# Optimization experiments

Hardware: AMD Instinct MI355X
Metric: run time of the kernel (lower is better)

Reference implementation:

```python
import jax, jax.numpy as jnp
import numpy as np
import math

B, D, S, H = 4, 1024, 2048, 16


def setup_inputs() -> dict:
    key = jax.random.key(0)
    ks = jax.random.split(key, 9)
    scale = 0.02
    return {
        "x": jax.random.normal(ks[0], (B, D, S), dtype=jnp.float32),
        "Wq": jax.random.normal(ks[1], (D, D), dtype=jnp.float32) * scale,
        "bq": jnp.zeros((D,), dtype=jnp.float32),
        "Wk": jax.random.normal(ks[2], (D, D), dtype=jnp.float32) * scale,
        "bk": jnp.zeros((D,), dtype=jnp.float32),
        "Wv": jax.random.normal(ks[3], (D, D), dtype=jnp.float32) * scale,
        "bv": jnp.zeros((D,), dtype=jnp.float32),
        "Wo": jax.random.normal(ks[4], (D, D), dtype=jnp.float32) * scale,
        "bo": jnp.zeros((D,), dtype=jnp.float32),
        "num_heads": H,
    }


def _positional_encoding(d_model, seq_len):
    # pe[0::2, :] = sin(pos * denom), pe[1::2, :] = cos(pos * denom)
    pos = jnp.arange(seq_len, dtype=jnp.float32)[None, :]            # [1, S]
    denom = jnp.exp(jnp.arange(0, d_model, 2, dtype=jnp.float32)
                    * (-math.log(10000.0) / d_model))[:, None]        # [D/2, 1]
    angles = pos * denom                                              # [D/2, S]
    pe = jnp.zeros((d_model, seq_len), dtype=jnp.float32)
    pe = pe.at[0::2, :].set(jnp.sin(angles))
    pe = pe.at[1::2, :].set(jnp.cos(angles))
    return pe


def reference(x, Wq, bq, Wk, bk, Wv, bv, Wo, bo, num_heads):
    b, d_model, s = x.shape
    head_dim = d_model // num_heads
    x = x + _positional_encoding(d_model, s)[None, :, :]  # broadcast over batch
    x = jnp.transpose(x, (0, 2, 1))                       # [B, S, D]
    q = x @ Wq.T + bq
    k = x @ Wk.T + bk
    v = x @ Wv.T + bv
    # [B, S, H, hd] -> [B, H, S, hd]
    q = q.reshape(b, s, num_heads, head_dim).transpose(0, 2, 1, 3)
    k = k.reshape(b, s, num_heads, head_dim).transpose(0, 2, 1, 3)
    v = v.reshape(b, s, num_heads, head_dim).transpose(0, 2, 1, 3)
    scores = jnp.einsum('bhqd,bhkd->bhqk', q, k) / jnp.sqrt(
        jnp.asarray(head_dim, dtype=jnp.float32))
    attn = jax.nn.softmax(scores, axis=-1)
    out = jnp.einsum('bhqk,bhkd->bhqd', attn, v)          # [B, H, S, hd]
    out = out.transpose(0, 2, 1, 3).reshape(b, s, d_model)
    out = out @ Wo.T + bo
    return jnp.transpose(out, (0, 2, 1))                  # [B, D, S]
```

## Files before the change

kernel.cpp:

```cpp
#include <hip/hip_runtime.h>


typedef __bf16 bf16;
typedef __attribute__((ext_vector_type(8))) __bf16 bf16x8;
typedef __attribute__((ext_vector_type(4))) __bf16 bf16x4;
typedef __attribute__((ext_vector_type(2))) __bf16 bf16x2;
typedef __attribute__((ext_vector_type(4))) float f32x4;
typedef __attribute__((ext_vector_type(2))) unsigned int uintx2;
typedef __attribute__((ext_vector_type(4))) unsigned int uintx4;

#define NB 4
#define ND 1024
#define NS 2048
#define NH 16
#define NM 8192

__device__ __forceinline__ void gld16(const void* g, void* l) {
  __builtin_amdgcn_global_load_lds((__attribute__((address_space(1))) void*)g,
                                   (__attribute__((address_space(3))) void*)l, 16, 0, 0);
}

__device__ __forceinline__ float exp2_fast(float x) {
#if __has_builtin(__builtin_amdgcn_exp2f)
  return __builtin_amdgcn_exp2f(x);
#else
  return exp2f(x);
#endif
}

__device__ __forceinline__ unsigned pk2(float a, float b) {
  bf16x2 t;
  t[0] = (bf16)a;
  t[1] = (bf16)b;
  return __builtin_bit_cast(unsigned int, t);
}

__device__ __forceinline__ void lane_xchg(unsigned a, unsigned b, unsigned& lo,
                                          unsigned& hi) {
#if __has_builtin(__builtin_amdgcn_permlane32_swap) && \
    __has_builtin(__builtin_amdgcn_permlane16_swap)
  uintx2 r = __builtin_amdgcn_permlane32_swap(a, b, false, false);
  uintx2 r2 = __builtin_amdgcn_permlane16_swap(r[0], r[1], false, false);
  lo = r2[0];
  hi = r2[1];
#else
  const int lane = threadIdx.x & 63;
  const int src = (lane & 15) + ((lane >> 4) & 1) * 32;
  const unsigned as = (unsigned)__shfl((int)a, src, 64);
  const unsigned bs = (unsigned)__shfl((int)b, src, 64);
  const unsigned as2 = (unsigned)__shfl((int)a, src + 16, 64);
  const unsigned bs2 = (unsigned)__shfl((int)b, src + 16, 64);
  lo = (lane >= 32) ? bs : as;
  hi = (lane >= 32) ? bs2 : as2;
#endif
}

__global__ __launch_bounds__(256) void prep_x_kernel(const float* __restrict__ x,
                                                     bf16* __restrict__ xT) {
  __shared__ float t[32][33];
  const int tx = threadIdx.x, ty = threadIdx.y;
  const int s0 = blockIdx.x * 32, d0 = blockIdx.y * 32, b = blockIdx.z;
#pragma unroll
  for (int i = 0; i < 4; ++i) {
    const int rr = ty + i * 8;
    const int d = d0 + rr, s = s0 + tx;
    const float freq = __expf(-(float)(d >> 1) * 0.01798894603980689f);
    const float ang = (float)s * freq;
    const float pe = (d & 1) ? cosf(ang) : sinf(ang);
    t[rr][tx] = x[((size_t)b * ND + d) * NS + s] + pe;
  }
  __syncthreads();
#pragma unroll
  for (int i = 0; i < 4; ++i) {
    const int a = ty + i * 8;
    xT[((size_t)b * NS + s0 + a) * ND + d0 + tx] = (bf16)t[tx][a];
  }
}

__global__ __launch_bounds__(256) void prep_w_kernel(const float* __restrict__ Wq,
                                                     const float* __restrict__ Wk,
                                                     const float* __restrict__ Wv,
                                                     const float* __restrict__ Wo,
                                                     bf16* __restrict__ Wqkv,
                                                     bf16* __restrict__ WoB) {
  const size_t t = (size_t)blockIdx.x * blockDim.x + threadIdx.x;
  const size_t i = t * 4;
  const float* src;
  bf16* dst;
  size_t off;
  if (i < (size_t)3 * 1024 * 1024) {
    const int sel = (int)(i >> 20);
    src = sel == 0 ? Wq : (sel == 1 ? Wk : Wv);
    off = i - ((size_t)sel << 20);
    dst = Wqkv + i;
  } else {
    src = Wo;
    off = i - ((size_t)3 << 20);
    dst = WoB + off;
  }
  const f32x4 v = *(const f32x4*)(src + off);
  bf16x4 o;
  o[0] = (bf16)v[0];
  o[1] = (bf16)v[1];
  o[2] = (bf16)v[2];
  o[3] = (bf16)v[3];
  *(bf16x4*)dst = o;
}

__device__ __forceinline__ void gemm_tile_128(const bf16* __restrict__ A,
                                              const bf16* __restrict__ Bm,
                                              int tm, int tn, bf16* ldsA, bf16* ldsB,
                                              f32x4 acc[4][4]) {
  const int tid = threadIdx.x;
  const int lane = tid & 63, wave = tid >> 6;
  const int wm = wave >> 1, wn = wave & 1;
  const int rl = lane & 15, quad = lane >> 4;
  int r0[4], c0[4];
#pragma unroll
  for (int j = 0; j < 4; ++j) {
    const int o = (wave * 4 + j) * 1024 + lane * 16;
    const int r = o >> 7;
    r0[j] = r;
    c0[j] = ((((o >> 4) & 7) ^ (r & 7)) * 8);
  }
  for (int kt = 0; kt < 1024; kt += 64) {
#pragma unroll
    for (int j = 0; j < 4; ++j) {
      gld16(A + (size_t)(tm + r0[j]) * 1024 + kt + c0[j], (char*)ldsA + (wave * 4 + j) * 1024);
      gld16(Bm + (size_t)(tn + r0[j]) * 1024 + kt + c0[j], (char*)ldsB + (wave * 4 + j) * 1024);
    }
    __syncthreads();
#pragma unroll
    for (int kk = 0; kk < 2; ++kk) {
      bf16x8 af[4], bfr[4];
#pragma unroll
      for (int i = 0; i < 4; ++i) {
        const int ra = wm * 64 + i * 16 + rl;
        af[i] = *(const bf16x8*)((const char*)ldsA + ra * 128 +
                                 (((kk * 4 + quad) ^ (rl & 7)) * 16));
        const int rb = wn * 64 + i * 16 + rl;
        bfr[i] = *(const bf16x8*)((const char*)ldsB + rb * 128 +
                                  (((kk * 4 + quad) ^ (rl & 7)) * 16));
      }
#pragma unroll
      for (int i = 0; i < 4; ++i)
#pragma unroll
        for (int j = 0; j < 4; ++j)
          acc[i][j] =
              __builtin_amdgcn_mfma_f32_16x16x32_bf16(af[i], bfr[j], acc[i][j], 0, 0, 0);
    }
    __syncthreads();
  }
}

__global__ __launch_bounds__(256, 2) void gemm_qkv_kernel(
    const bf16* __restrict__ xT, const bf16* __restrict__ Wqkv,
    const float* __restrict__ bq, const float* __restrict__ bk,
    const float* __restrict__ bv, bf16* __restrict__ Q, bf16* __restrict__ Kb,
    bf16* __restrict__ VT) {
  __shared__ bf16 ldsA[128 * 64], ldsB[128 * 64];
  const int tm = blockIdx.x * 128, tn = blockIdx.y * 128;
  f32x4 acc[4][4];
  const f32x4 z = {0.f, 0.f, 0.f, 0.f};
#pragma unroll
  for (int i = 0; i < 4; ++i)
#pragma unroll
    for (int j = 0; j < 4; ++j) acc[i][j] = z;
  gemm_tile_128(xT, Wqkv, tm, tn, ldsA, ldsB, acc);
  const int lane = threadIdx.x & 63, wave = threadIdx.x >> 6;
  const int wm = wave >> 1, wn = wave & 1;
  const int rl = lane & 15, quad = lane >> 4;
  const float QSCALE = 0.18033688011112042f;
#pragma unroll
  for (int j = 0; j < 4; ++j) {
    const int n = tn + wn * 64 + j * 16 + rl;
    const int which = n >> 10;
    const int nl = n & 1023;
    const int h = nl >> 6, d = nl & 63;
    const float bias = (which == 0 ? bq : which == 1 ? bk : bv)[nl];
#pragma unroll
    for (int i = 0; i < 4; ++i) {
      const int m0 = tm + wm * 64 + i * 16 + quad * 4;
      const int b = m0 >> 11, s0 = m0 & 2047;
      const size_t bh = (size_t)(b * 16 + h);
      if (which == 2) {
        bf16x4 pk;
#pragma unroll
        for (int r = 0; r < 4; ++r) pk[r] = (bf16)(acc[i][j][r] + bias);
        *(bf16x4*)(VT + ((size_t)bh * 64 + d) * 2048 + s0) = pk;
      } else {
#pragma unroll
        for (int r = 0; r < 4; ++r) {
          const float v = acc[i][j][r] + bias;
          const int s = s0 + r;
          if (which == 0)
            Q[(bh * 2048 + s) * 64 + d] = (bf16)(v * QSCALE);
          else
            Kb[(bh * 2048 + s) * 64 + d] = (bf16)v;
        }
      }
    }
  }
}

__global__ __launch_bounds__(256, 4) void attn_kernel(const bf16* __restrict__ Q,
                                                      const bf16* __restrict__ Kb,
                                                      const bf16* __restrict__ VT,
                                                      bf16* __restrict__ AO) {
  __shared__ __align__(16) char smem[32768];
  char* ldsK = smem;
  char* ldsV = smem + 16384;
  const int tid = threadIdx.x;
  const int lane = tid & 63, wave = tid >> 6;
  const int rl = lane & 15, quad = lane >> 4;
  const int bh = blockIdx.x;
  const int q0 = blockIdx.y * 128;
  const bf16* Qb = Q + ((size_t)bh * 2048 + q0) * 64;
  const bf16* Kbb = Kb + (size_t)bh * 2048 * 64;
  const bf16* Vb = VT + (size_t)bh * 64 * 2048;
  const int o0 = wave * 1024 + lane * 16, o1 = o0 + 4096;
  const int ra = o0 >> 7, rb = o1 >> 7;
  const int ca = (((o0 >> 4) & 7) ^ (ra & 7)) * 16;
  const int cb = (((o1 >> 4) & 7) ^ (rb & 7)) * 16;
  gld16((const char*)Kbb + (size_t)ra * 128 + ca, ldsK + wave * 1024);
  gld16((const char*)Kbb + (size_t)rb * 128 + cb, ldsK + wave * 1024 + 4096);
  gld16((const char*)Vb + (size_t)ra * 4096 + ca, ldsV + wave * 1024);
  gld16((const char*)Vb + (size_t)rb * 4096 + cb, ldsV + wave * 1024 + 4096);
  bf16x8 qf[2][2];
#pragma unroll
  for (int i = 0; i < 2; ++i)
#pragma unroll
    for (int ks = 0; ks < 2; ++ks)
      qf[i][ks] =
          *(const bf16x8*)(Qb + (wave * 32 + i * 16 + rl) * 64 + ks * 32 + quad * 8);
  f32x4 o_acc[2][4], lacc[2];
  const f32x4 z = {0.f, 0.f, 0.f, 0.f};
#pragma unroll
  for (int i = 0; i < 2; ++i) {
    lacc[i] = z;
#pragma unroll
    for (int j = 0; j < 4; ++j) o_acc[i][j] = z;
  }
  const bf16 oneb = (bf16)1.0f;
  const bf16x8 onesb = {oneb, oneb, oneb, oneb, oneb, oneb, oneb, oneb};
  const int kcol0 = (quad ^ (rl & 7)) * 16 + rl * 128;
  const int kcol1 = ((4 + quad) ^ (rl & 7)) * 16 + rl * 128;
  const int ksr = wave & 1;
  int ksOff[2], vcol[2];
#pragma unroll
  for (int ksi = 0; ksi < 2; ++ksi) {
    const int ks = ksi ^ ksr;
    ksOff[ksi] = ks * 4096;
    vcol[ksi] = ((ks * 4 + quad) ^ (rl & 7)) * 16 + rl * 128;
  }
  int buf = 0;
  for (int kt = 0; kt < 2048; kt += 64, buf ^= 1) {
    __syncthreads();
    if (kt + 64 < 2048) {
      const int nb = (buf ^ 1) * 8192;
      gld16((const char*)Kbb + (size_t)(kt + 64 + ra) * 128 + ca, ldsK + nb + wave * 1024);
      gld16((const char*)Kbb + (size_t)(kt + 64 + rb) * 128 + cb,
            ldsK + nb + wave * 1024 + 4096);
      gld16((const char*)Vb + (size_t)ra * 4096 + (size_t)(kt + 64) * 2 + ca,
            ldsV + nb + wave * 1024);
      gld16((const char*)Vb + (size_t)rb * 4096 + (size_t)(kt + 64) * 2 + cb,
            ldsV + nb + wave * 1024 + 4096);
    }
    const char* Kbase = ldsK + buf * 8192;
    const char* Vbase = ldsV + buf * 8192;
#pragma unroll
    for (int ksi = 0; ksi < 2; ++ksi) {
      const bf16x8 k00 = *(const bf16x8*)(Kbase + ksOff[ksi] + kcol0);
      const bf16x8 k01 = *(const bf16x8*)(Kbase + ksOff[ksi] + kcol1);
      const bf16x8 k10 = *(const bf16x8*)(Kbase + ksOff[ksi] + 2048 + kcol0);
      const bf16x8 k11 = *(const bf16x8*)(Kbase + ksOff[ksi] + 2048 + kcol1);
      f32x4 s[2][2];
      __builtin_amdgcn_s_setprio(1);
#pragma unroll
      for (int i = 0; i < 2; ++i) {
        s[i][0] = __builtin_amdgcn_mfma_f32_16x16x32_bf16(k00, qf[i][0], z, 0, 0, 0);
        s[i][0] = __builtin_amdgcn_mfma_f32_16x16x32_bf16(k01, qf[i][1], s[i][0], 0, 0, 0);
        s[i][1] = __builtin_amdgcn_mfma_f32_16x16x32_bf16(k10, qf[i][0], z, 0, 0, 0);
        s[i][1] = __builtin_amdgcn_mfma_f32_16x16x32_bf16(k11, qf[i][1], s[i][1], 0, 0, 0);
      }
      __builtin_amdgcn_s_setprio(0);
      bf16x8 vf[4];
#pragma unroll
      for (int j = 0; j < 4; ++j)
        vf[j] = *(const bf16x8*)(Vbase + j * 2048 + vcol[ksi]);
#pragma unroll
      for (int i = 0; i < 2; ++i) {
        const unsigned a0 = pk2(exp2_fast(s[i][0][0]), exp2_fast(s[i][0][1]));
        const unsigned a1 = pk2(exp2_fast(s[i][0][2]), exp2_fast(s[i][0][3]));
        const unsigned b0 = pk2(exp2_fast(s[i][1][0]), exp2_fast(s[i][1][1]));
        const unsigned b1 = pk2(exp2_fast(s[i][1][2]), exp2_fast(s[i][1][3]));
        unsigned d0, d1, d2, d3;
        lane_xchg(a0, b0, d0, d2);
        lane_xchg(a1, b1, d1, d3);
        uintx4 dd;
        dd[0] = d0;
        dd[1] = d1;
        dd[2] = d2;
        dd[3] = d3;
        const bf16x8 pf = __builtin_bit_cast(bf16x8, dd);
        __builtin_amdgcn_s_setprio(1);
        lacc[i] =
            __builtin_amdgcn_mfma_f32_16x16x32_bf16(pf, onesb, lacc[i], 0, 0, 0);
#pragma unroll
        for (int j = 0; j < 4; ++j)
          o_acc[i][j] =
              __builtin_amdgcn_mfma_f32_16x16x32_bf16(pf, vf[j], o_acc[i][j], 0, 0, 0);
        __builtin_amdgcn_s_setprio(0);
      }
    }
  }
  const int b = bh >> 4, h = bh & 15;
#pragma unroll
  for (int i = 0; i < 2; ++i) {
    f32x4 linv;
#pragma unroll
    for (int r = 0; r < 4; ++r) linv[r] = __builtin_amdgcn_rcpf(lacc[i][r]);
#pragma unroll
    for (int j = 0; j < 4; ++j)
#pragma unroll
      for (int r = 0; r < 4; ++r) {
        const int s = q0 + wave * 32 + i * 16 + quad * 4 + r;
        const int d = h * 64 + j * 16 + rl;
        AO[((size_t)b * 2048 + s) * 1024 + d] = (bf16)(o_acc[i][j][r] * linv[r]);
      }
  }
}

__global__ __launch_bounds__(256, 2) void gemm_out_kernel(const bf16* __restrict__ AO,
                                                          const bf16* __restrict__ WoB,
                                                          const float* __restrict__ bo,
                                                          float* __restrict__ out) {
  __shared__ bf16 ldsA[128 * 64], ldsB[128 * 64];
  const int tm = blockIdx.x * 128, tn = blockIdx.y * 128;
  f32x4 acc[4][4];
  const f32x4 z = {0.f, 0.f, 0.f, 0.f};
#pragma unroll
  for (int i = 0; i < 4; ++i)
#pragma unroll
    for (int j = 0; j < 4; ++j) acc[i][j] = z;
  gemm_tile_128(AO, WoB, tm, tn, ldsA, ldsB, acc);
  const int lane = threadIdx.x & 63, wave = threadIdx.x >> 6;
  const int wm = wave >> 1, wn = wave & 1;
  const int rl = lane & 15, quad = lane >> 4;
#pragma unroll
  for (int j = 0; j < 4; ++j) {
    const int n = tn + wn * 64 + j * 16 + rl;
    const float bias = bo[n];
#pragma unroll
    for (int i = 0; i < 4; ++i) {
      const int m0 = tm + wm * 64 + i * 16 + quad * 4;
      const int b = m0 >> 11, s = m0 & 2047;
      f32x4 v = acc[i][j];
      v[0] += bias;
      v[1] += bias;
      v[2] += bias;
      v[3] += bias;
      *(f32x4*)(out + ((size_t)(b * 1024 + n)) * 2048 + s) = v;
    }
  }
}

extern "C" void kernel_launch(void* const* d_in, const int* in_sizes, int n_in,
                              void* d_out, int out_size, void* d_ws, size_t ws_size,
                              hipStream_t stream) {
  const float* x = (const float*)d_in[0];
  const float* Wq = (const float*)d_in[1];
  const float* bq = (const float*)d_in[2];
  const float* Wk = (const float*)d_in[3];
  const float* bk = (const float*)d_in[4];
  const float* Wv = (const float*)d_in[5];
  const float* bv = (const float*)d_in[6];
  const float* Wo = (const float*)d_in[7];
  const float* bo = (const float*)d_in[8];
  float* out = (float*)d_out;

  char* p = (char*)d_ws;
  bf16* xT = (bf16*)p;
  p += (size_t)NM * ND * 2;
  bf16* Wqkv = (bf16*)p;
  p += (size_t)3 * ND * ND * 2;
  bf16* WoB = (bf16*)p;
  p += (size_t)ND * ND * 2;
  bf16* Qb = (bf16*)p;
  p += (size_t)NM * ND * 2;
  bf16* Kbf = (bf16*)p;
  p += (size_t)NM * ND * 2;
  bf16* VTb = (bf16*)p;
  p += (size_t)NM * ND * 2;
  bf16* AO = xT;

  prep_x_kernel<<<dim3(NS / 32, ND / 32, NB), dim3(32, 8), 0, stream>>>(x, xT);
  prep_w_kernel<<<dim3(4096), dim3(256), 0, stream>>>(Wq, Wk, Wv, Wo, Wqkv, WoB);
  gemm_qkv_kernel<<<dim3(NM / 128, 3072 / 128), dim3(256), 0, stream>>>(
      xT, Wqkv, bq, bk, bv, Qb, Kbf, VTb);
  attn_kernel<<<dim3(NB * NH, NS / 128), dim3(256), 0, stream>>>(Qb, Kbf, VTb, AO);
  gemm_out_kernel<<<dim3(NM / 128, ND / 128), dim3(256), 0, stream>>>(AO, WoB, bo, out);
}
```

Baseline: 262.3 us.

## Software-pipeline attention loop to overlap QK MFMA with exp and PV

Restructures the attention inner loop into a skewed software pipeline. Each 64-key tile is split into two 32-key halves, and the QK product of one half is interleaved with the exp/pack and PV of the previous half. sched_group_barrier hints interleave MFMA with VALU work, and the LDS refill is moved to sit between the two barriers of each iteration. Launch bounds drop from 4 to 3 blocks per CU so the extra live score/fragment registers fit, at the cost of occupancy. The per-wave k-half swizzle and the setprio calls are removed.

```diff
diff --git a/kernel.cpp b/kernel.cpp
--- a/kernel.cpp
+++ b/kernel.cpp
@@ -203,7 +203,7 @@
   }
 }
 
-__global__ __launch_bounds__(256, 4) void attn_kernel(const bf16* __restrict__ Q,
+__global__ __launch_bounds__(256, 3) void attn_kernel(const bf16* __restrict__ Q,
                                                       const bf16* __restrict__ Kb,
                                                       const bf16* __restrict__ VT,
                                                       bf16* __restrict__ AO) {
@@ -222,10 +222,15 @@
   const int ra = o0 >> 7, rb = o1 >> 7;
   const int ca = (((o0 >> 4) & 7) ^ (ra & 7)) * 16;
   const int cb = (((o1 >> 4) & 7) ^ (rb & 7)) * 16;
-  gld16((const char*)Kbb + (size_t)ra * 128 + ca, ldsK + wave * 1024);
-  gld16((const char*)Kbb + (size_t)rb * 128 + cb, ldsK + wave * 1024 + 4096);
-  gld16((const char*)Vb + (size_t)ra * 4096 + ca, ldsV + wave * 1024);
-  gld16((const char*)Vb + (size_t)rb * 4096 + cb, ldsV + wave * 1024 + 4096);
+  auto stage = [&](int tn, int nb) {
+    gld16((const char*)Kbb + (size_t)(tn * 64 + ra) * 128 + ca, ldsK + nb + wave * 1024);
+    gld16((const char*)Kbb + (size_t)(tn * 64 + rb) * 128 + cb,
+          ldsK + nb + wave * 1024 + 4096);
+    gld16((const char*)Vb + (size_t)ra * 4096 + tn * 128 + ca, ldsV + nb + wave * 1024);
+    gld16((const char*)Vb + (size_t)rb * 4096 + tn * 128 + cb,
+          ldsV + nb + wave * 1024 + 4096);
+  };
+  stage(0, 0);
   bf16x8 qf[2][2];
 #pragma unroll
   for (int i = 0; i < 2; ++i)
@@ -243,77 +248,97 @@
   }
   const bf16 oneb = (bf16)1.0f;
   const bf16x8 onesb = {oneb, oneb, oneb, oneb, oneb, oneb, oneb, oneb};
-  const int kcol0 = (quad ^ (rl & 7)) * 16 + rl * 128;
-  const int kcol1 = ((4 + quad) ^ (rl & 7)) * 16 + rl * 128;
-  const int ksr = wave & 1;
-  int ksOff[2], vcol[2];
-#pragma unroll
-  for (int ksi = 0; ksi < 2; ++ksi) {
-    const int ks = ksi ^ ksr;
-    ksOff[ksi] = ks * 4096;
-    vcol[ksi] = ((ks * 4 + quad) ^ (rl & 7)) * 16 + rl * 128;
-  }
-  int buf = 0;
-  for (int kt = 0; kt < 2048; kt += 64, buf ^= 1) {
+  const int xa = (quad ^ (rl & 7)) * 16;
+  const int xb = ((4 + quad) ^ (rl & 7)) * 16;
+  auto qk_half = [&](const char* Kbase, int h, f32x4(&s)[2][2]) {
+    const int r0o = (h * 32 + rl) * 128, r1o = (h * 32 + 16 + rl) * 128;
+    const bf16x8 k00 = *(const bf16x8*)(Kbase + r0o + xa);
+    const bf16x8 k01 = *(const bf16x8*)(Kbase + r0o + xb);
+    const bf16x8 k10 = *(const bf16x8*)(Kbase + r1o + xa);
+    const bf16x8 k11 = *(const bf16x8*)(Kbase + r1o + xb);
+#pragma unroll
+    for (int i = 0; i < 2; ++i) {
+      s[i][0] = __builtin_amdgcn_mfma_f32_16x16x32_bf16(k00, qf[i][0], z, 0, 0, 0);
+      s[i][0] = __builtin_amdgcn_mfma_f32_16x16x32_bf16(k01, qf[i][1], s[i][0], 0, 0, 0);
+      s[i][1] = __builtin_amdgcn_mfma_f32_16x16x32_bf16(k10, qf[i][0], z, 0, 0, 0);
+      s[i][1] = __builtin_amdgcn_mfma_f32_16x16x32_bf16(k11, qf[i][1], s[i][1], 0, 0, 0);
+    }
+  };
+  auto exppack = [&](const f32x4(&s)[2][2], bf16x8(&pf)[2]) {
+#pragma unroll
+    for (int i = 0; i < 2; ++i) {
+      const unsigned a0 = pk2(exp2_fast(s[i][0][0]), exp2_fast(s[i][0][1]));
+      const unsigned a1 = pk2(exp2_fast(s[i][0][2]), exp2_fast(s[i][0][3]));
+      const unsigned b0 = pk2(exp2_fast(s[i][1][0]), exp2_fast(s[i][1][1]));
+      const unsigned b1 = pk2(exp2_fast(s[i][1][2]), exp2_fast(s[i][1][3]));
+      unsigned d0, d1, d2, d3;
+      lane_xchg(a0, b0, d0, d2);
+      lane_xchg(a1, b1, d1, d3);
+      uintx4 dd;
+      dd[0] = d0;
+      dd[1] = d1;
+      dd[2] = d2;
+      dd[3] = d3;
+      pf[i] = __builtin_bit_cast(bf16x8, dd);
+    }
+  };
+  auto ldv = [&](const char* Vbase, int h, bf16x8(&vf)[4]) {
+    const int vc = ((h * 4 + quad) ^ (rl & 7)) * 16;
+#pragma unroll
+    for (int j = 0; j < 4; ++j)
+      vf[j] = *(const bf16x8*)(Vbase + (j * 16 + rl) * 128 + vc);
+  };
+  auto pv = [&](const bf16x8(&pf)[2], const bf16x8(&vf)[4]) {
+#pragma unroll
+    for (int i = 0; i < 2; ++i)
+      lacc[i] = __builtin_amdgcn_mfma_f32_16x16x32_bf16(pf[i], onesb, lacc[i], 0, 0, 0);
+#pragma unroll
+    for (int j = 0; j < 4; ++j)
+#pragma unroll
+      for (int i = 0; i < 2; ++i)
+        o_acc[i][j] =
+            __builtin_amdgcn_mfma_f32_16x16x32_bf16(pf[i], vf[j], o_acc[i][j], 0, 0, 0);
+  };
+  f32x4 sh0[2][2], sh1[2][2];
+  bf16x8 pf0[2], pf1[2], vf0[4], vf1[4];
+  __syncthreads();
+  stage(1, 8192);
+  qk_half(ldsK, 0, sh0);
+  exppack(sh0, pf0);
+  ldv(ldsV, 0, vf0);
+  pv(pf0, vf0);
+  qk_half(ldsK, 1, sh1);
+  for (int t = 1; t < 32; ++t) {
+    const char* KbT = ldsK + (t & 1) * 8192;
+    const char* VbT = ldsV + (t & 1) * 8192;
+    const char* VbO = ldsV + ((t & 1) ^ 1) * 8192;
     __syncthreads();
-    if (kt + 64 < 2048) {
-      const int nb = (buf ^ 1) * 8192;
-      gld16((const char*)Kbb + (size_t)(kt + 64 + ra) * 128 + ca, ldsK + nb + wave * 1024);
-      gld16((const char*)Kbb + (size_t)(kt + 64 + rb) * 128 + cb,
-            ldsK + nb + wave * 1024 + 4096);
-      gld16((const char*)Vb + (size_t)ra * 4096 + (size_t)(kt + 64) * 2 + ca,
-            ldsV + nb + wave * 1024);
-      gld16((const char*)Vb + (size_t)rb * 4096 + (size_t)(kt + 64) * 2 + cb,
-            ldsV + nb + wave * 1024 + 4096);
-    }
-    const char* Kbase = ldsK + buf * 8192;
-    const char* Vbase = ldsV + buf * 8192;
-#pragma unroll
-    for (int ksi = 0; ksi < 2; ++ksi) {
-      const bf16x8 k00 = *(const bf16x8*)(Kbase + ksOff[ksi] + kcol0);
-      const bf16x8 k01 = *(const bf16x8*)(Kbase + ksOff[ksi] + kcol1);
-      const bf16x8 k10 = *(const bf16x8*)(Kbase + ksOff[ksi] + 2048 + kcol0);
-      const bf16x8 k11 = *(const bf16x8*)(Kbase + ksOff[ksi] + 2048 + kcol1);
-      f32x4 s[2][2];
-      __builtin_amdgcn_s_setprio(1);
-#pragma unroll
-      for (int i = 0; i < 2; ++i) {
-        s[i][0] = __builtin_amdgcn_mfma_f32_16x16x32_bf16(k00, qf[i][0], z, 0, 0, 0);
-        s[i][0] = __builtin_amdgcn_mfma_f32_16x16x32_bf16(k01, qf[i][1], s[i][0], 0, 0, 0);
-        s[i][1] = __builtin_amdgcn_mfma_f32_16x16x32_bf16(k10, qf[i][0], z, 0, 0, 0);
-        s[i][1] = __builtin_amdgcn_mfma_f32_16x16x32_bf16(k11, qf[i][1], s[i][1], 0, 0, 0);
-      }
-      __builtin_amdgcn_s_setprio(0);
-      bf16x8 vf[4];
-#pragma unroll
-      for (int j = 0; j < 4; ++j)
-        vf[j] = *(const bf16x8*)(Vbase + j * 2048 + vcol[ksi]);
-#pragma unroll
-      for (int i = 0; i < 2; ++i) {
-        const unsigned a0 = pk2(exp2_fast(s[i][0][0]), exp2_fast(s[i][0][1]));
-        const unsigned a1 = pk2(exp2_fast(s[i][0][2]), exp2_fast(s[i][0][3]));
-        const unsigned b0 = pk2(exp2_fast(s[i][1][0]), exp2_fast(s[i][1][1]));
-        const unsigned b1 = pk2(exp2_fast(s[i][1][2]), exp2_fast(s[i][1][3]));
-        unsigned d0, d1, d2, d3;
-        lane_xchg(a0, b0, d0, d2);
-        lane_xchg(a1, b1, d1, d3);
-        uintx4 dd;
-        dd[0] = d0;
-        dd[1] = d1;
-        dd[2] = d2;
-        dd[3] = d3;
-        const bf16x8 pf = __builtin_bit_cast(bf16x8, dd);
-        __builtin_amdgcn_s_setprio(1);
-        lacc[i] =
-            __builtin_amdgcn_mfma_f32_16x16x32_bf16(pf, onesb, lacc[i], 0, 0, 0);
-#pragma unroll
-        for (int j = 0; j < 4; ++j)
-          o_acc[i][j] =
-              __builtin_amdgcn_mfma_f32_16x16x32_bf16(pf, vf[j], o_acc[i][j], 0, 0, 0);
-        __builtin_amdgcn_s_setprio(0);
-      }
-    }
-  }
+    ldv(VbO, 1, vf1);
+    qk_half(KbT, 0, sh0);
+    exppack(sh1, pf1);
+#pragma unroll
+    for (int g = 0; g < 8; ++g) {
+      __builtin_amdgcn_sched_group_barrier(0x008, 1, 0);
+      __builtin_amdgcn_sched_group_barrier(0x002, 5, 0);
+    }
+    if (t < 31) {
+      __syncthreads();
+      stage(t + 1, ((t & 1) ^ 1) * 8192);
+    }
+    pv(pf1, vf1);
+    qk_half(KbT, 1, sh1);
+    exppack(sh0, pf0);
+#pragma unroll
+    for (int g = 0; g < 18; ++g) {
+      __builtin_amdgcn_sched_group_barrier(0x008, 1, 0);
+      __builtin_amdgcn_sched_group_barrier(0x002, 2, 0);
+    }
+    ldv(VbT, 0, vf0);
+    pv(pf0, vf0);
+  }
+  exppack(sh1, pf1);
+  ldv(ldsV + 8192, 1, vf1);
+  pv(pf1, vf1);
   const int b = bh >> 4, h = bh & 15;
 #pragma unroll
   for (int i = 0; i < 2; ++i) {
```

Measured after the change: 256.9 us. 1.02x faster.
